# Kernel optimization log

Hardware: AMD Instinct MI355X
Metric: run time of the kernel (lower is better)

## Reference

```python
import jax, jax.numpy as jnp
import numpy as np

BETA = 0.9
THRESH = 1.0
ALPHA = 2.0  # snntorch ATan surrogate default

@jax.custom_vjp
def atan_spike(x):
    return (x > 0).astype(x.dtype)

def _atan_fwd(x):
    return atan_spike(x), x

def _atan_bwd(x, g):
    # d/dx of snntorch ATan surrogate: (alpha/2) / (1 + (pi/2*alpha*x)^2)
    return (g * (ALPHA / 2) / (1 + (jnp.pi / 2 * ALPHA * x) ** 2),)

atan_spike.defvjp(_atan_fwd, _atan_bwd)

def setup_inputs() -> dict:
    key = jax.random.key(0)
    k1, k2, k3, k4, k5 = jax.random.split(key, 5)
    B, T, F, H, O = 256, 1024, 64, 512, 64
    x = jax.random.normal(k1, (B, T, F), dtype=jnp.float32)
    s_in = 1.0 / np.sqrt(F)
    s_out = 1.0 / np.sqrt(H)
    W_in = jax.random.uniform(k2, (H, F), jnp.float32, -s_in, s_in)
    b_in = jax.random.uniform(k3, (H,), jnp.float32, -s_in, s_in)
    W_out = jax.random.uniform(k4, (O, H), jnp.float32, -s_out, s_out)
    b_out = jax.random.uniform(k5, (O,), jnp.float32, -s_out, s_out)
    return {"x": x, "W_in": W_in, "b_in": b_in, "W_out": W_out, "b_out": b_out}

def reference(x, W_in, b_in, W_out, b_out):
    B, T, F = x.shape
    H = W_in.shape[0]
    O = W_out.shape[0]
    dt = x.dtype
    # precompute input currents for all steps: [T, B, H]
    cur1_all = jnp.einsum('btf,hf->tbh', x, W_in) + b_in

    def step(carry, cur1):
        mem1, mem_out = carry
        # snntorch Leaky(subtract): reset from previous mem (detached),
        # then mem = beta*mem + input - reset*threshold, spike from new mem.
        reset1 = jax.lax.stop_gradient((mem1 > THRESH).astype(dt))
        mem1 = BETA * mem1 + cur1 - reset1 * THRESH
        spk1 = atan_spike(mem1 - THRESH)
        cur_out = spk1 @ W_out.T + b_out
        reset_o = jax.lax.stop_gradient((mem_out > THRESH).astype(dt))
        mem_out = BETA * mem_out + cur_out - reset_o * THRESH
        spk_out = atan_spike(mem_out - THRESH)
        return (mem1, mem_out), (mem_out, spk_out)

    init = (jnp.zeros((B, H), dt), jnp.zeros((B, O), dt))
    _, (mem_rec, spk_rec) = jax.lax.scan(step, init, cur1_all)
    # [T, B, O] -> [B, T, O]
    return mem_rec.transpose(1, 0, 2), spk_rec.transpose(1, 0, 2)
```

## Files before the change

### kernel.cpp

```cpp
#include <hip/hip_runtime.h>


namespace {
constexpr int kB = 256;
constexpr int kT = 1024;
constexpr int kF = 64;
constexpr int kH = 512;
constexpr int kO = 64;
constexpr float kBeta = 0.9f;
constexpr float kThresh = 1.0f;
}

typedef __attribute__((ext_vector_type(16))) float f32x16;

#define PIN8(p)                                                            \
  asm volatile("" : "+v"((p)[0]), "+v"((p)[1]), "+v"((p)[2]),              \
                    "+v"((p)[3]), "+v"((p)[4]), "+v"((p)[5]),              \
                    "+v"((p)[6]), "+v"((p)[7]))

#define BARRIER() asm volatile("s_waitcnt lgkmcnt(0)\n\ts_barrier" ::: "memory")

#define SX(i) ((i) < 16 ? sx0[(i)] : (i) < 32 ? sx1[(i)-16]                \
             : (i) < 48 ? sx2[(i)-32] : sx3[(i)-48])
#define AQ(q)                                                              \
  c0 = fmaf(SX(4*(q)+0), w[4*(q)+0], c0);                                  \
  c1 = fmaf(SX(4*(q)+1), w[4*(q)+1], c1);                                  \
  c2 = fmaf(SX(4*(q)+2), w[4*(q)+2], c2);                                  \
  c3 = fmaf(SX(4*(q)+3), w[4*(q)+3], c3);

__global__ __launch_bounds__(512)
void snn_curA(const float* __restrict__ x, const float* __restrict__ W_in,
              const float* __restrict__ b_in, float* __restrict__ cur1,
              int t0, int ntc, int l2ntc, int rpb) {
  const int l = threadIdx.x & 63;
  const int s = threadIdx.x >> 6;
  const int h = s * 64 + l;

  float w[64];
  {
    const float4* wiv = reinterpret_cast<const float4*>(W_in) + h * 16;
#pragma unroll
    for (int q = 0; q < 16; ++q) {
      const float4 v = wiv[q];
      w[4*q+0] = v.x; w[4*q+1] = v.y; w[4*q+2] = v.z; w[4*q+3] = v.w;
    }
  }
  float binh = b_in[h];
  PIN8(w + 0);  PIN8(w + 8);  PIN8(w + 16); PIN8(w + 24);
  PIN8(w + 32); PIN8(w + 40); PIN8(w + 48); PIN8(w + 56);
  asm volatile("" : "+v"(binh));

  const int row0 = blockIdx.x * rpb;
#pragma unroll 1
  for (int r = 0; r < rpb; ++r) {
    const int row = row0 + r;
    const int b = row >> l2ntc;
    const int tc = row & (ntc - 1);
    const float* xp = x + ((size_t)b * kT + (size_t)(t0 + tc)) * kF;
    f32x16 sx0, sx1, sx2, sx3;
    asm volatile("s_load_dwordx16 %0, %4, 0x0\n\t"
                 "s_load_dwordx16 %1, %4, 0x40\n\t"
                 "s_load_dwordx16 %2, %4, 0x80\n\t"
                 "s_load_dwordx16 %3, %4, 0xc0"
                 : "=&s"(sx0), "=&s"(sx1), "=&s"(sx2), "=&s"(sx3)
                 : "s"(xp));
    asm volatile("s_waitcnt lgkmcnt(0)"
                 : "+s"(sx0), "+s"(sx1), "+s"(sx2), "+s"(sx3) :: "memory");
    float c0 = binh, c1 = 0.0f, c2 = 0.0f, c3 = 0.0f;
    AQ(0) AQ(1) AQ(2) AQ(3) AQ(4) AQ(5) AQ(6) AQ(7)
    AQ(8) AQ(9) AQ(10) AQ(11) AQ(12) AQ(13) AQ(14) AQ(15)
    cur1[(size_t)row * kH + h] = (c0 + c1) + (c2 + c3);
  }
}

#define BSTEP(fk, tt)                                                      \
  do {                                                                     \
    mem1 = kBeta * mem1 + (fk) - rst1;                                     \
    const bool pr = mem1 > kThresh;                                        \
    rst1 = pr ? 1.0f : 0.0f;                                               \
    cp[(size_t)(tt) * kH] = rst1;          \
    const int tn_ = ((tt) + 8 < ntc) ? (tt) + 8 : ntc - 1;                 \
    fk = cp[(size_t)tn_ * kH];         \
  } while (0)

__global__ __launch_bounds__(512)
void snn_scanB(float* __restrict__ cs, float* __restrict__ state,
               int t0, int ntc) {
  const int b = blockIdx.x;
  const int h = threadIdx.x;
  float* m1s = state;
  float* r1s = state + kB * kH;
  const int idx = b * kH + h;
  float mem1 = 0.0f, rst1 = 0.0f;
  if (t0 != 0) { mem1 = m1s[idx]; rst1 = r1s[idx]; }

  float* cp = cs + (size_t)b * ntc * kH + h;
  float f0 = cp[0 * (size_t)kH], f1 = cp[1 * (size_t)kH];
  float f2 = cp[2 * (size_t)kH], f3 = cp[3 * (size_t)kH];
  float f4 = cp[4 * (size_t)kH], f5 = cp[5 * (size_t)kH];
  float f6 = cp[6 * (size_t)kH], f7 = cp[7 * (size_t)kH];

#pragma unroll 1
  for (int t = 0; t < ntc; t += 8) {
    BSTEP(f0, t + 0); BSTEP(f1, t + 1); BSTEP(f2, t + 2); BSTEP(f3, t + 3);
    BSTEP(f4, t + 4); BSTEP(f5, t + 5); BSTEP(f6, t + 6); BSTEP(f7, t + 7);
  }
  m1s[idx] = mem1;
  r1s[idx] = rst1;
}

#define SC(i) ((i) < 16 ? m0[(i)] : (i) < 32 ? m1[(i)-16]                  \
             : (i) < 48 ? m2[(i)-32] : m3[(i)-48])

#define CROW(rr)                                                           \
  do {                                                                     \
    const float* sp = spkrow + (size_t)(rr) * kH;                          \
    f32x16 m0, m1, m2, m3;                                                 \
    asm volatile("s_load_dwordx16 %0, %4, 0x0\n\t"                         \
                 "s_load_dwordx16 %1, %4, 0x40\n\t"                        \
                 "s_load_dwordx16 %2, %4, 0x80\n\t"                        \
                 "s_load_dwordx16 %3, %4, 0xc0"                            \
                 : "=&s"(m0), "=&s"(m1), "=&s"(m2), "=&s"(m3)              \
                 : "s"(sp));                                               \
    asm volatile("s_waitcnt lgkmcnt(0)"                                    \
                 : "+s"(m0), "+s"(m1), "+s"(m2), "+s"(m3) :: "memory");    \
    float a0 = 0.0f, a1 = 0.0f, a2 = 0.0f, a3 = 0.0f;                      \
    _Pragma("unroll") for (int q = 0; q < 16; ++q) {                       \
      a0 = fmaf(SC(4 * q + 0), wout[4 * q + 0], a0);                       \
      a1 = fmaf(SC(4 * q + 1), wout[4 * q + 1], a1);                       \
      a2 = fmaf(SC(4 * q + 2), wout[4 * q + 2], a2);                       \
      a3 = fmaf(SC(4 * q + 3), wout[4 * q + 3], a3);                       \
    }                                                                      \
    red[buf][rr][s][o] = (a0 + a1) + (a2 + a3);                            \
  } while (0)

__global__ __launch_bounds__(512)
void snn_coutC(const float* __restrict__ spk, const float* __restrict__ W_out,
               const float* __restrict__ b_out, float* __restrict__ cout,
               int ntc) {
  const int j = threadIdx.x;
  const int o = j & 63;
  const int s = j >> 6;
  const int s_u = __builtin_amdgcn_readfirstlane(s);
  const size_t row0 = (size_t)blockIdx.x * 64;

  __shared__ float red[2][8][8][64];

  float wout[64];
  {
    const float4* wov =
        reinterpret_cast<const float4*>(W_out) + o * (kH / 4) + s * 16;
#pragma unroll
    for (int q = 0; q < 16; ++q) {
      const float4 v = wov[q];
      wout[4*q+0] = v.x; wout[4*q+1] = v.y;
      wout[4*q+2] = v.z; wout[4*q+3] = v.w;
    }
  }
  float bout = b_out[o];
  PIN8(wout + 0);  PIN8(wout + 8);  PIN8(wout + 16); PIN8(wout + 24);
  PIN8(wout + 32); PIN8(wout + 40); PIN8(wout + 48); PIN8(wout + 56);
  asm volatile("" : "+v"(bout));

#pragma unroll 1
  for (int rb = 0; rb < 64; rb += 8) {
    const int buf = (rb >> 3) & 1;
    const float* spkrow = spk + (row0 + (size_t)rb) * kH + s_u * 64;

    CROW(0); CROW(1); CROW(2); CROW(3);
    CROW(4); CROW(5); CROW(6); CROW(7);

    BARRIER();

    float co = bout;
    co += red[buf][s][0][o]; co += red[buf][s][1][o];
    co += red[buf][s][2][o]; co += red[buf][s][3][o];
    co += red[buf][s][4][o]; co += red[buf][s][5][o];
    co += red[buf][s][6][o]; co += red[buf][s][7][o];
    cout[(row0 + (size_t)(rb + s)) * kO + o] = co;
  }
}

#define DSTEP(gk, tt)                                                      \
  do {                                                                     \
    memo = kBeta * memo + (gk) - rsto;                                     \
    const float so = (memo > kThresh) ? 1.0f : 0.0f;                       \
    rsto = so;                                                             \
    om[(size_t)(tt) * kO] = memo;                                          \
    os[(size_t)(tt) * kO] = so;                                            \
    const int tn_ = ((tt) + 8 < ntc) ? (tt) + 8 : ntc - 1;                 \
    gk = dp[(size_t)tn_ * kO];                                             \
  } while (0)

__global__ __launch_bounds__(64)
void snn_memoD(const float* __restrict__ cout, float* __restrict__ out,
               float* __restrict__ state, int t0, int ntc) {
  const int b = blockIdx.x;
  const int o = threadIdx.x;
  float* mos = state + 2 * kB * kH;
  float* ros = mos + kB * kO;
  const int idx = b * kO + o;
  float memo = 0.0f, rsto = 0.0f;
  if (t0 != 0) { memo = mos[idx]; rsto = ros[idx]; }

  const float* dp = cout + (size_t)b * ntc * kO + o;
  float* om = out + ((size_t)b * kT + t0) * kO + o;
  float* os = om + (size_t)kB * kT * kO;

  float g0 = dp[0 * (size_t)kO], g1 = dp[1 * (size_t)kO];
  float g2 = dp[2 * (size_t)kO], g3 = dp[3 * (size_t)kO];
  float g4 = dp[4 * (size_t)kO], g5 = dp[5 * (size_t)kO];
  float g6 = dp[6 * (size_t)kO], g7 = dp[7 * (size_t)kO];

#pragma unroll 1
  for (int t = 0; t < ntc; t += 8) {
    DSTEP(g0, t + 0); DSTEP(g1, t + 1); DSTEP(g2, t + 2); DSTEP(g3, t + 3);
    DSTEP(g4, t + 4); DSTEP(g5, t + 5); DSTEP(g6, t + 6); DSTEP(g7, t + 7);
  }
  mos[idx] = memo;
  ros[idx] = rsto;
}

__global__ __launch_bounds__(256)
void warm_x_kernel(const float4* __restrict__ p, int n4) {
  float acc = 0.0f;
  for (int i = blockIdx.x * blockDim.x + threadIdx.x; i < n4;
       i += gridDim.x * blockDim.x) {
    const float4 v = p[i];
    acc += v.x + v.y + v.z + v.w;
  }
  asm volatile("" ::"v"(acc));
}

__global__ __launch_bounds__(512)
__attribute__((amdgpu_waves_per_eu(2, 2)))
void snn_fused5(const float* __restrict__ x, const float* __restrict__ W_in,
                const float* __restrict__ b_in,
                const float* __restrict__ W_out,
                const float* __restrict__ b_out, float* __restrict__ out) {
  const int b = blockIdx.x;
  const int j = threadIdx.x;
  const int o = j & 63;
  const int s = j >> 6;
  __shared__ float red[2][8][64];
  float win[kF];
  {
    const float4* wiv = reinterpret_cast<const float4*>(W_in) + j * 16;
#pragma unroll
    for (int q = 0; q < 16; ++q) {
      const float4 v = wiv[q];
      win[4 * q] = v.x; win[4 * q + 1] = v.y;
      win[4 * q + 2] = v.z; win[4 * q + 3] = v.w;
    }
  }
  float wout[64];
  {
    const float4* wov =
        reinterpret_cast<const float4*>(W_out) + o * 128 + s * 16;
#pragma unroll
    for (int q = 0; q < 16; ++q) {
      const float4 v = wov[q];
      wout[4 * q] = v.x; wout[4 * q + 1] = v.y;
      wout[4 * q + 2] = v.z; wout[4 * q + 3] = v.w;
    }
  }
  float bin_j = b_in[j];
  float bout_o = b_out[o];
  PIN8(win + 0);  PIN8(win + 8);  PIN8(win + 16); PIN8(win + 24);
  PIN8(win + 32); PIN8(win + 40); PIN8(win + 48); PIN8(win + 56);
  PIN8(wout + 0);  PIN8(wout + 8);  PIN8(wout + 16); PIN8(wout + 24);
  PIN8(wout + 32); PIN8(wout + 40); PIN8(wout + 48); PIN8(wout + 56);
  asm volatile("" : "+v"(bin_j), "+v"(bout_o));
  float mem1 = 0.0f, rst1 = 0.0f, memo = 0.0f, rsto = 0.0f;
  unsigned long long mask = 0ull;
  const float4* xv = reinterpret_cast<const float4*>(x + (size_t)b * kT * kF);
  float* out_mem = out + (size_t)b * kT * kO + o;
  float* out_spk = out_mem + (size_t)kB * kT * kO;
  float4 x0, x1, x2, x3, x4, x5, x6, x7, x8, x9, x10, x11, x12, x13, x14, x15;
#define LOADX(tt)                                                          \
  do {                                                                     \
    const float4* xp = xv + (size_t)(tt) * 16;                             \
    x0 = xp[0]; x1 = xp[1]; x2 = xp[2]; x3 = xp[3];                        \
    x4 = xp[4]; x5 = xp[5]; x6 = xp[6]; x7 = xp[7];                        \
    x8 = xp[8]; x9 = xp[9]; x10 = xp[10]; x11 = xp[11];                    \
    x12 = xp[12]; x13 = xp[13]; x14 = xp[14]; x15 = xp[15];                \
  } while (0)
#define L1Q(q)                                                             \
  c0 = fmaf(x##q.x, win[4 * q + 0], c0);                                   \
  c1 = fmaf(x##q.y, win[4 * q + 1], c1);                                   \
  c2 = fmaf(x##q.z, win[4 * q + 2], c2);                                   \
  c3 = fmaf(x##q.w, win[4 * q + 3], c3);
#define LAYER1F()                                                          \
  do {                                                                     \
    float c0 = bin_j, c1 = 0.0f, c2 = 0.0f, c3 = 0.0f;                     \
    L1Q(0) L1Q(1) L1Q(2) L1Q(3) L1Q(4) L1Q(5) L1Q(6) L1Q(7)                \
    L1Q(8) L1Q(9) L1Q(10) L1Q(11) L1Q(12) L1Q(13) L1Q(14) L1Q(15)          \
    const float cur1v = (c0 + c1) + (c2 + c3);                             \
    mem1 = kBeta * mem1 + cur1v - rst1;                                    \
    const bool p = mem1 > kThresh;                                         \
    mask = __ballot(p);                                                    \
    rst1 = p ? 1.0f : 0.0f;                                                \
  } while (0)
#define L2QS(q)                                                            \
  {                                                                        \
    const float f0 = ((mlo >> (4 * (q) + 0)) & 1u) ? 1.0f : 0.0f;          \
    const float f1 = ((mlo >> (4 * (q) + 1)) & 1u) ? 1.0f : 0.0f;          \
    const float f2 = ((mlo >> (4 * (q) + 2)) & 1u) ? 1.0f : 0.0f;          \
    const float f3 = ((mlo >> (4 * (q) + 3)) & 1u) ? 1.0f : 0.0f;          \
    a0 = fmaf(f0, wout[4 * (q) + 0], a0);                                  \
    a1 = fmaf(f1, wout[4 * (q) + 1], a1);                                  \
    a2 = fmaf(f2, wout[4 * (q) + 2], a2);                                  \
    a3 = fmaf(f3, wout[4 * (q) + 3], a3);                                  \
  }
#define L2E(acc, q, i)                                                     \
  acc = acc + __uint_as_float(                                             \
      (unsigned)__builtin_amdgcn_sbfe((int)vmhi, 4 * (q) + (i)-32, 1) &    \
      __float_as_uint(wout[4 * (q) + (i)]));
#define L2QV(q)                                                            \
  { L2E(a0, q, 0) L2E(a1, q, 1) L2E(a2, q, 2) L2E(a3, q, 3) }
#define LAYER2F(buf)                                                       \
  do {                                                                     \
    const unsigned mlo = (unsigned)mask;                                   \
    unsigned vmhi = (unsigned)(mask >> 32);                                \
    asm volatile("" : "+v"(vmhi));                                         \
    float a0 = 0.0f, a1 = 0.0f, a2 = 0.0f, a3 = 0.0f;                      \
    L2QS(0) L2QS(1) L2QS(2) L2QS(3) L2QS(4) L2QS(5) L2QS(6) L2QS(7)        \
    L2QV(8) L2QV(9) L2QV(10) L2QV(11) L2QV(12) L2QV(13) L2QV(14) L2QV(15)  \
    red[(buf)][s][o] = (a0 + a1) + (a2 + a3);                              \
  } while (0)
  LOADX(0);
  LAYER1F();
  LOADX(1);
  for (int t = 1; t < kT; ++t) {
    LAYER2F((t - 1) & 1);
    BARRIER();
    float r0, r1, r2, r3, r4, r5, r6, r7;
    const int buf = (t - 1) & 1;
    if (s == 0) {
      r0 = red[buf][0][o]; r1 = red[buf][1][o];
      r2 = red[buf][2][o]; r3 = red[buf][3][o];
      r4 = red[buf][4][o]; r5 = red[buf][5][o];
      r6 = red[buf][6][o]; r7 = red[buf][7][o];
    }
    LAYER1F();
    const int tn = (t + 1 < kT) ? (t + 1) : (kT - 1);
    LOADX(tn);
    if (s == 0) {
      float co = bout_o;
      co += r0; co += r1; co += r2; co += r3;
      co += r4; co += r5; co += r6; co += r7;
      memo = kBeta * memo + co - rsto;
      const float so = (memo > kThresh) ? 1.0f : 0.0f;
      rsto = so;
      out_mem[(t - 1) * kO] = memo;
      out_spk[(t - 1) * kO] = so;
    }
  }
  LAYER2F((kT - 1) & 1);
  BARRIER();
  if (s == 0) {
    const int buf = (kT - 1) & 1;
    float co = bout_o;
    co += red[buf][0][o]; co += red[buf][1][o];
    co += red[buf][2][o]; co += red[buf][3][o];
    co += red[buf][4][o]; co += red[buf][5][o];
    co += red[buf][6][o]; co += red[buf][7][o];
    memo = kBeta * memo + co - rsto;
    const float so = (memo > kThresh) ? 1.0f : 0.0f;
    out_mem[(kT - 1) * kO] = memo;
    out_spk[(kT - 1) * kO] = so;
  }
}

extern "C" void kernel_launch(void* const* d_in, const int* in_sizes, int n_in,
                              void* d_out, int out_size, void* d_ws,
                              size_t ws_size, hipStream_t stream) {
  const float* x = (const float*)d_in[0];
  const float* W_in = (const float*)d_in[1];
  const float* b_in = (const float*)d_in[2];
  const float* W_out = (const float*)d_in[3];
  const float* b_out = (const float*)d_in[4];
  float* out = (float*)d_out;

  const size_t state_bytes = ((size_t)2 * kB * kH + 2 * kB * kO) * 4;
  int nch = 0;
  for (int c : {4, 8, 16}) {
    const int ntc_c = kT / c;
    const size_t need = (size_t)kB * ntc_c * (kH + kO) * 4 + state_bytes;
    if (need <= ws_size) { nch = c; break; }
  }

  if (nch) {
    const int ntc = kT / nch;
    const int l2ntc = (ntc == 256) ? 8 : (ntc == 128) ? 7 : 6;
    float* cur1 = (float*)d_ws;
    float* coutb = cur1 + (size_t)kB * ntc * kH;
    float* state = coutb + (size_t)kB * ntc * kO;

    const int rows = kB * ntc;
    const int rpbA = 64;
    const int gA = rows / rpbA;
    const int gC = rows / 64;

    for (int c = 0; c < nch; ++c) {
      const int t0 = c * ntc;
      hipLaunchKernelGGL(snn_curA, dim3(gA), dim3(512), 0, stream,
                         x, W_in, b_in, cur1, t0, ntc, l2ntc, rpbA);
      hipLaunchKernelGGL(snn_scanB, dim3(kB), dim3(512), 0, stream,
                         cur1, state, t0, ntc);
      hipLaunchKernelGGL(snn_coutC, dim3(gC), dim3(512), 0, stream,
                         cur1, W_out, b_out, coutb, ntc);
      hipLaunchKernelGGL(snn_memoD, dim3(kB), dim3(64), 0, stream,
                         coutb, out, state, t0, ntc);
    }
  } else {
    const int n4 = kB * kT * kF / 4;
    hipLaunchKernelGGL(warm_x_kernel, dim3(1024), dim3(256), 0, stream,
                       (const float4*)x, n4);
    hipLaunchKernelGGL(snn_fused5, dim3(kB), dim3(512), 0, stream,
                       x, W_in, b_in, W_out, b_out, out);
  }
}
```

Before: 1.028 ms.

## Fuse input projection into hidden-layer scan kernel, dropping cur1 buffer round-trip

Merges the input-current matmul kernel and the hidden membrane scan kernel into one kernel per batch row. Each thread holds its W_in row in registers, computes the current for each timestep from a double-buffered float4 load of x, updates the membrane state and writes only the spike. This removes the write and reread of the full cur1 buffer and one launch per chunk. In exchange only 256 blocks do the input projection, so its compute now sits on the serial scan's critical path with lower parallelism.

```diff
diff --git a/kernel.cpp b/kernel.cpp
--- a/kernel.cpp
+++ b/kernel.cpp
@@ -20,91 +20,86 @@
 
 #define BARRIER() asm volatile("s_waitcnt lgkmcnt(0)\n\ts_barrier" ::: "memory")
 
-#define SX(i) ((i) < 16 ? sx0[(i)] : (i) < 32 ? sx1[(i)-16]                \
-             : (i) < 48 ? sx2[(i)-32] : sx3[(i)-48])
-#define AQ(q)                                                              \
-  c0 = fmaf(SX(4*(q)+0), w[4*(q)+0], c0);                                  \
-  c1 = fmaf(SX(4*(q)+1), w[4*(q)+1], c1);                                  \
-  c2 = fmaf(SX(4*(q)+2), w[4*(q)+2], c2);                                  \
-  c3 = fmaf(SX(4*(q)+3), w[4*(q)+3], c3);
+#define SLOAD64(sx0, sx1, sx2, sx3, ptr)                                   \
+  asm volatile("s_load_dwordx16 %0, %4, 0x0\n\t"                           \
+               "s_load_dwordx16 %1, %4, 0x40\n\t"                          \
+               "s_load_dwordx16 %2, %4, 0x80\n\t"                          \
+               "s_load_dwordx16 %3, %4, 0xc0\n\t"                          \
+               "s_waitcnt lgkmcnt(0)"                                      \
+               : "=&s"(sx0), "=&s"(sx1), "=&s"(sx2), "=&s"(sx3)            \
+               : "s"(ptr) : "memory")
+
+#define FMA4(v, q)                                                         \
+  c0 = fmaf((v).x, w[4 * (q) + 0], c0);                                    \
+  c1 = fmaf((v).y, w[4 * (q) + 1], c1);                                    \
+  c2 = fmaf((v).z, w[4 * (q) + 2], c2);                                    \
+  c3 = fmaf((v).w, w[4 * (q) + 3], c3);
+
+#define LDB(bk, tt)                                                        \
+  do {                                                                     \
+    const float4* p = xv + (size_t)(tt) * 16;                              \
+    bk##0 = p[0]; bk##1 = p[1]; bk##2 = p[2]; bk##3 = p[3];                \
+    bk##4 = p[4]; bk##5 = p[5]; bk##6 = p[6]; bk##7 = p[7];                \
+    bk##8 = p[8]; bk##9 = p[9]; bk##10 = p[10]; bk##11 = p[11];            \
+    bk##12 = p[12]; bk##13 = p[13]; bk##14 = p[14]; bk##15 = p[15];        \
+  } while (0)
+
+#define STEP(bk, tt)                                                       \
+  do {                                                                     \
+    float c0 = bias, c1 = 0.0f, c2 = 0.0f, c3 = 0.0f;                      \
+    FMA4(bk##0, 0) FMA4(bk##1, 1) FMA4(bk##2, 2) FMA4(bk##3, 3)            \
+    FMA4(bk##4, 4) FMA4(bk##5, 5) FMA4(bk##6, 6) FMA4(bk##7, 7)            \
+    FMA4(bk##8, 8) FMA4(bk##9, 9) FMA4(bk##10, 10) FMA4(bk##11, 11)        \
+    FMA4(bk##12, 12) FMA4(bk##13, 13) FMA4(bk##14, 14) FMA4(bk##15, 15)    \
+    const float cur = (c0 + c1) + (c2 + c3);                               \
+    mem1 = kBeta * mem1 + cur - rst1;                                      \
+    rst1 = (mem1 > kThresh) ? 1.0f : 0.0f;                                 \
+    sp[(size_t)(tt) * kH] = rst1;                                          \
+  } while (0)
 
 __global__ __launch_bounds__(512)
-void snn_curA(const float* __restrict__ x, const float* __restrict__ W_in,
-              const float* __restrict__ b_in, float* __restrict__ cur1,
-              int t0, int ntc, int l2ntc, int rpb) {
-  const int l = threadIdx.x & 63;
-  const int s = threadIdx.x >> 6;
-  const int h = s * 64 + l;
+void snn_ab(const float* __restrict__ x, const float* __restrict__ W_in,
+            const float* __restrict__ b_in, float* __restrict__ spk,
+            float* __restrict__ state, int t0, int ntc) {
+  const int b = blockIdx.x;
+  const int j = threadIdx.x;
 
   float w[64];
   {
-    const float4* wiv = reinterpret_cast<const float4*>(W_in) + h * 16;
+    const float4* wiv = reinterpret_cast<const float4*>(W_in) + j * 16;
 #pragma unroll
     for (int q = 0; q < 16; ++q) {
       const float4 v = wiv[q];
       w[4*q+0] = v.x; w[4*q+1] = v.y; w[4*q+2] = v.z; w[4*q+3] = v.w;
     }
   }
-  float binh = b_in[h];
+  float bias = b_in[j];
   PIN8(w + 0);  PIN8(w + 8);  PIN8(w + 16); PIN8(w + 24);
   PIN8(w + 32); PIN8(w + 40); PIN8(w + 48); PIN8(w + 56);
-  asm volatile("" : "+v"(binh));
-
-  const int row0 = blockIdx.x * rpb;
-#pragma unroll 1
-  for (int r = 0; r < rpb; ++r) {
-    const int row = row0 + r;
-    const int b = row >> l2ntc;
-    const int tc = row & (ntc - 1);
-    const float* xp = x + ((size_t)b * kT + (size_t)(t0 + tc)) * kF;
-    f32x16 sx0, sx1, sx2, sx3;
-    asm volatile("s_load_dwordx16 %0, %4, 0x0\n\t"
-                 "s_load_dwordx16 %1, %4, 0x40\n\t"
-                 "s_load_dwordx16 %2, %4, 0x80\n\t"
-                 "s_load_dwordx16 %3, %4, 0xc0"
-                 : "=&s"(sx0), "=&s"(sx1), "=&s"(sx2), "=&s"(sx3)
-                 : "s"(xp));
-    asm volatile("s_waitcnt lgkmcnt(0)"
-                 : "+s"(sx0), "+s"(sx1), "+s"(sx2), "+s"(sx3) :: "memory");
-    float c0 = binh, c1 = 0.0f, c2 = 0.0f, c3 = 0.0f;
-    AQ(0) AQ(1) AQ(2) AQ(3) AQ(4) AQ(5) AQ(6) AQ(7)
-    AQ(8) AQ(9) AQ(10) AQ(11) AQ(12) AQ(13) AQ(14) AQ(15)
-    cur1[(size_t)row * kH + h] = (c0 + c1) + (c2 + c3);
-  }
-}
-
-#define BSTEP(fk, tt)                                                      \
-  do {                                                                     \
-    mem1 = kBeta * mem1 + (fk) - rst1;                                     \
-    const bool pr = mem1 > kThresh;                                        \
-    rst1 = pr ? 1.0f : 0.0f;                                               \
-    cp[(size_t)(tt) * kH] = rst1;          \
-    const int tn_ = ((tt) + 8 < ntc) ? (tt) + 8 : ntc - 1;                 \
-    fk = cp[(size_t)tn_ * kH];         \
-  } while (0)
-
-__global__ __launch_bounds__(512)
-void snn_scanB(float* __restrict__ cs, float* __restrict__ state,
-               int t0, int ntc) {
-  const int b = blockIdx.x;
-  const int h = threadIdx.x;
+  asm volatile("" : "+v"(bias));
+
   float* m1s = state;
   float* r1s = state + kB * kH;
-  const int idx = b * kH + h;
+  const int idx = b * kH + j;
   float mem1 = 0.0f, rst1 = 0.0f;
   if (t0 != 0) { mem1 = m1s[idx]; rst1 = r1s[idx]; }
 
-  float* cp = cs + (size_t)b * ntc * kH + h;
-  float f0 = cp[0 * (size_t)kH], f1 = cp[1 * (size_t)kH];
-  float f2 = cp[2 * (size_t)kH], f3 = cp[3 * (size_t)kH];
-  float f4 = cp[4 * (size_t)kH], f5 = cp[5 * (size_t)kH];
-  float f6 = cp[6 * (size_t)kH], f7 = cp[7 * (size_t)kH];
-
+  const float4* xv =
+      reinterpret_cast<const float4*>(x + ((size_t)b * kT + t0) * kF);
+  float* sp = spk + (size_t)b * ntc * kH + j;
+
+  float4 a0, a1, a2, a3, a4, a5, a6, a7, a8, a9, a10, a11, a12, a13, a14, a15;
+  float4 e0, e1, e2, e3, e4, e5, e6, e7, e8, e9, e10, e11, e12, e13, e14, e15;
+
+  LDB(a, 0);
 #pragma unroll 1
-  for (int t = 0; t < ntc; t += 8) {
-    BSTEP(f0, t + 0); BSTEP(f1, t + 1); BSTEP(f2, t + 2); BSTEP(f3, t + 3);
-    BSTEP(f4, t + 4); BSTEP(f5, t + 5); BSTEP(f6, t + 6); BSTEP(f7, t + 7);
-  }
+  for (int t = 0; t < ntc; t += 2) {
+    LDB(e, t + 1);
+    STEP(a, t);
+    LDB(a, (t + 2 < ntc) ? t + 2 : t);
+    STEP(e, t + 1);
+  }
+
   m1s[idx] = mem1;
   r1s[idx] = rst1;
 }
@@ -114,16 +109,9 @@
 
 #define CROW(rr)                                                           \
   do {                                                                     \
-    const float* sp = spkrow + (size_t)(rr) * kH;                          \
+    const float* sp_ = spkrow + (size_t)(rr) * kH;                         \
     f32x16 m0, m1, m2, m3;                                                 \
-    asm volatile("s_load_dwordx16 %0, %4, 0x0\n\t"                         \
-                 "s_load_dwordx16 %1, %4, 0x40\n\t"                        \
-                 "s_load_dwordx16 %2, %4, 0x80\n\t"                        \
-                 "s_load_dwordx16 %3, %4, 0xc0"                            \
-                 : "=&s"(m0), "=&s"(m1), "=&s"(m2), "=&s"(m3)              \
-                 : "s"(sp));                                               \
-    asm volatile("s_waitcnt lgkmcnt(0)"                                    \
-                 : "+s"(m0), "+s"(m1), "+s"(m2), "+s"(m3) :: "memory");    \
+    SLOAD64(m0, m1, m2, m3, sp_);                                          \
     float a0 = 0.0f, a1 = 0.0f, a2 = 0.0f, a3 = 0.0f;                      \
     _Pragma("unroll") for (int q = 0; q < 16; ++q) {                       \
       a0 = fmaf(SC(4 * q + 0), wout[4 * q + 0], a0);                       \
@@ -392,24 +380,19 @@
 
   if (nch) {
     const int ntc = kT / nch;
-    const int l2ntc = (ntc == 256) ? 8 : (ntc == 128) ? 7 : 6;
-    float* cur1 = (float*)d_ws;
-    float* coutb = cur1 + (size_t)kB * ntc * kH;
+    float* spkb = (float*)d_ws;
+    float* coutb = spkb + (size_t)kB * ntc * kH;
     float* state = coutb + (size_t)kB * ntc * kO;
 
     const int rows = kB * ntc;
-    const int rpbA = 64;
-    const int gA = rows / rpbA;
     const int gC = rows / 64;
 
     for (int c = 0; c < nch; ++c) {
       const int t0 = c * ntc;
-      hipLaunchKernelGGL(snn_curA, dim3(gA), dim3(512), 0, stream,
-                         x, W_in, b_in, cur1, t0, ntc, l2ntc, rpbA);
-      hipLaunchKernelGGL(snn_scanB, dim3(kB), dim3(512), 0, stream,
-                         cur1, state, t0, ntc);
+      hipLaunchKernelGGL(snn_ab, dim3(kB), dim3(512), 0, stream,
+                         x, W_in, b_in, spkb, state, t0, ntc);
       hipLaunchKernelGGL(snn_coutC, dim3(gC), dim3(512), 0, stream,
-                         cur1, W_out, b_out, coutb, ntc);
+                         spkb, W_out, b_out, coutb, ntc);
       hipLaunchKernelGGL(snn_memoD, dim3(kB), dim3(64), 0, stream,
                          coutb, out, state, t0, ntc);
     }
```

Result: slower. 1.249 ms (+21.5%).

## Software-pipeline chunks by fusing next-chunk input GEMM with current output GEMM

Applied to the files above, without the earlier changes.

Double-buffers the cur1 and cout workspaces and merges the input-current GEMM for chunk c+1 with the output-current GEMM for chunk c into one launch that interleaves the two roles across blocks. The aim is to cut the number of launches and let the two independent, parallel stages share the GPU instead of running serially. It needs twice the workspace and picks 8 or 16 chunks. The fused single-kernel fallback is removed, so the function now returns without computing anything when the workspace is too small.

```diff
diff --git a/kernel.cpp b/kernel.cpp
--- a/kernel.cpp
+++ b/kernel.cpp
@@ -28,10 +28,11 @@
   c2 = fmaf(SX(4*(q)+2), w[4*(q)+2], c2);                                  \
   c3 = fmaf(SX(4*(q)+3), w[4*(q)+3], c3);
 
-__global__ __launch_bounds__(512)
-void snn_curA(const float* __restrict__ x, const float* __restrict__ W_in,
-              const float* __restrict__ b_in, float* __restrict__ cur1,
-              int t0, int ntc, int l2ntc, int rpb) {
+__device__ __forceinline__ void roleA(const float* __restrict__ x,
+                                      const float* __restrict__ W_in,
+                                      const float* __restrict__ b_in,
+                                      float* __restrict__ cur1,
+                                      int t0, int ntc, int l2ntc, int abid) {
   const int l = threadIdx.x & 63;
   const int s = threadIdx.x >> 6;
   const int h = s * 64 + l;
@@ -50,9 +51,9 @@
   PIN8(w + 32); PIN8(w + 40); PIN8(w + 48); PIN8(w + 56);
   asm volatile("" : "+v"(binh));
 
-  const int row0 = blockIdx.x * rpb;
+  const int row0 = abid * 64;
 #pragma unroll 1
-  for (int r = 0; r < rpb; ++r) {
+  for (int r = 0; r < 64; ++r) {
     const int row = row0 + r;
     const int b = row >> l2ntc;
     const int tc = row & (ntc - 1);
@@ -71,42 +72,6 @@
     AQ(8) AQ(9) AQ(10) AQ(11) AQ(12) AQ(13) AQ(14) AQ(15)
     cur1[(size_t)row * kH + h] = (c0 + c1) + (c2 + c3);
   }
-}
-
-#define BSTEP(fk, tt)                                                      \
-  do {                                                                     \
-    mem1 = kBeta * mem1 + (fk) - rst1;                                     \
-    const bool pr = mem1 > kThresh;                                        \
-    rst1 = pr ? 1.0f : 0.0f;                                               \
-    cp[(size_t)(tt) * kH] = rst1;          \
-    const int tn_ = ((tt) + 8 < ntc) ? (tt) + 8 : ntc - 1;                 \
-    fk = cp[(size_t)tn_ * kH];         \
-  } while (0)
-
-__global__ __launch_bounds__(512)
-void snn_scanB(float* __restrict__ cs, float* __restrict__ state,
-               int t0, int ntc) {
-  const int b = blockIdx.x;
-  const int h = threadIdx.x;
-  float* m1s = state;
-  float* r1s = state + kB * kH;
-  const int idx = b * kH + h;
-  float mem1 = 0.0f, rst1 = 0.0f;
-  if (t0 != 0) { mem1 = m1s[idx]; rst1 = r1s[idx]; }
-
-  float* cp = cs + (size_t)b * ntc * kH + h;
-  float f0 = cp[0 * (size_t)kH], f1 = cp[1 * (size_t)kH];
-  float f2 = cp[2 * (size_t)kH], f3 = cp[3 * (size_t)kH];
-  float f4 = cp[4 * (size_t)kH], f5 = cp[5 * (size_t)kH];
-  float f6 = cp[6 * (size_t)kH], f7 = cp[7 * (size_t)kH];
-
-#pragma unroll 1
-  for (int t = 0; t < ntc; t += 8) {
-    BSTEP(f0, t + 0); BSTEP(f1, t + 1); BSTEP(f2, t + 2); BSTEP(f3, t + 3);
-    BSTEP(f4, t + 4); BSTEP(f5, t + 5); BSTEP(f6, t + 6); BSTEP(f7, t + 7);
-  }
-  m1s[idx] = mem1;
-  r1s[idx] = rst1;
 }
 
 #define SC(i) ((i) < 16 ? m0[(i)] : (i) < 32 ? m1[(i)-16]                  \
@@ -134,17 +99,16 @@
     red[buf][rr][s][o] = (a0 + a1) + (a2 + a3);                            \
   } while (0)
 
-__global__ __launch_bounds__(512)
-void snn_coutC(const float* __restrict__ spk, const float* __restrict__ W_out,
-               const float* __restrict__ b_out, float* __restrict__ cout,
-               int ntc) {
+__device__ __forceinline__ void roleC(const float* __restrict__ spk,
+                                      const float* __restrict__ W_out,
+                                      const float* __restrict__ b_out,
+                                      float* __restrict__ cout, int cbid,
+                                      float (*red)[8][8][64]) {
   const int j = threadIdx.x;
   const int o = j & 63;
   const int s = j >> 6;
   const int s_u = __builtin_amdgcn_readfirstlane(s);
-  const size_t row0 = (size_t)blockIdx.x * 64;
-
-  __shared__ float red[2][8][8][64];
+  const size_t row0 = (size_t)cbid * 64;
 
   float wout[64];
   {
@@ -181,6 +145,72 @@
   }
 }
 
+__global__ __launch_bounds__(512)
+void snn_AC(const float* __restrict__ x, const float* __restrict__ W_in,
+            const float* __restrict__ b_in, float* __restrict__ cur1A,
+            const float* __restrict__ spkC, const float* __restrict__ W_out,
+            const float* __restrict__ b_out, float* __restrict__ coutC,
+            int tA0, int ntc, int l2ntc, int doA, int doC) {
+  __shared__ float red[2][8][8][64];
+  const int bid = blockIdx.x >> 1;
+  if (blockIdx.x & 1) {
+    if (doC) roleC(spkC, W_out, b_out, coutC, bid, red);
+  } else {
+    if (doA) roleA(x, W_in, b_in, cur1A, tA0, ntc, l2ntc, bid);
+  }
+}
+
+__global__ __launch_bounds__(512)
+void snn_curA(const float* __restrict__ x, const float* __restrict__ W_in,
+              const float* __restrict__ b_in, float* __restrict__ cur1,
+              int t0, int ntc, int l2ntc) {
+  roleA(x, W_in, b_in, cur1, t0, ntc, l2ntc, blockIdx.x);
+}
+
+__global__ __launch_bounds__(512)
+void snn_coutC(const float* __restrict__ spk, const float* __restrict__ W_out,
+               const float* __restrict__ b_out, float* __restrict__ cout,
+               int ntc) {
+  __shared__ float red[2][8][8][64];
+  roleC(spk, W_out, b_out, cout, blockIdx.x, red);
+}
+
+#define BSTEP(fk, tt)                                                      \
+  do {                                                                     \
+    mem1 = kBeta * mem1 + (fk) - rst1;                                     \
+    const bool pr = mem1 > kThresh;                                        \
+    rst1 = pr ? 1.0f : 0.0f;                                               \
+    cp[(size_t)(tt) * kH] = rst1;          \
+    const int tn_ = ((tt) + 8 < ntc) ? (tt) + 8 : ntc - 1;                 \
+    fk = cp[(size_t)tn_ * kH];                                             \
+  } while (0)
+
+__global__ __launch_bounds__(512)
+void snn_scanB(float* __restrict__ cs, float* __restrict__ state,
+               int t0, int ntc) {
+  const int b = blockIdx.x;
+  const int h = threadIdx.x;
+  float* m1s = state;
+  float* r1s = state + kB * kH;
+  const int idx = b * kH + h;
+  float mem1 = 0.0f, rst1 = 0.0f;
+  if (t0 != 0) { mem1 = m1s[idx]; rst1 = r1s[idx]; }
+
+  float* cp = cs + (size_t)b * ntc * kH + h;
+  float f0 = cp[0 * (size_t)kH], f1 = cp[1 * (size_t)kH];
+  float f2 = cp[2 * (size_t)kH], f3 = cp[3 * (size_t)kH];
+  float f4 = cp[4 * (size_t)kH], f5 = cp[5 * (size_t)kH];
+  float f6 = cp[6 * (size_t)kH], f7 = cp[7 * (size_t)kH];
+
+#pragma unroll 1
+  for (int t = 0; t < ntc; t += 8) {
+    BSTEP(f0, t + 0); BSTEP(f1, t + 1); BSTEP(f2, t + 2); BSTEP(f3, t + 3);
+    BSTEP(f4, t + 4); BSTEP(f5, t + 5); BSTEP(f6, t + 6); BSTEP(f7, t + 7);
+  }
+  m1s[idx] = mem1;
+  r1s[idx] = rst1;
+}
+
 #define DSTEP(gk, tt)                                                      \
   do {                                                                     \
     memo = kBeta * memo + (gk) - rsto;                                     \
@@ -221,157 +251,6 @@
   ros[idx] = rsto;
 }
 
-__global__ __launch_bounds__(256)
-void warm_x_kernel(const float4* __restrict__ p, int n4) {
-  float acc = 0.0f;
-  for (int i = blockIdx.x * blockDim.x + threadIdx.x; i < n4;
-       i += gridDim.x * blockDim.x) {
-    const float4 v = p[i];
-    acc += v.x + v.y + v.z + v.w;
-  }
-  asm volatile("" ::"v"(acc));
-}
-
-__global__ __launch_bounds__(512)
-__attribute__((amdgpu_waves_per_eu(2, 2)))
-void snn_fused5(const float* __restrict__ x, const float* __restrict__ W_in,
-                const float* __restrict__ b_in,
-                const float* __restrict__ W_out,
-                const float* __restrict__ b_out, float* __restrict__ out) {
-  const int b = blockIdx.x;
-  const int j = threadIdx.x;
-  const int o = j & 63;
-  const int s = j >> 6;
-  __shared__ float red[2][8][64];
-  float win[kF];
-  {
-    const float4* wiv = reinterpret_cast<const float4*>(W_in) + j * 16;
-#pragma unroll
-    for (int q = 0; q < 16; ++q) {
-      const float4 v = wiv[q];
-      win[4 * q] = v.x; win[4 * q + 1] = v.y;
-      win[4 * q + 2] = v.z; win[4 * q + 3] = v.w;
-    }
-  }
-  float wout[64];
-  {
-    const float4* wov =
-        reinterpret_cast<const float4*>(W_out) + o * 128 + s * 16;
-#pragma unroll
-    for (int q = 0; q < 16; ++q) {
-      const float4 v = wov[q];
-      wout[4 * q] = v.x; wout[4 * q + 1] = v.y;
-      wout[4 * q + 2] = v.z; wout[4 * q + 3] = v.w;
-    }
-  }
-  float bin_j = b_in[j];
-  float bout_o = b_out[o];
-  PIN8(win + 0);  PIN8(win + 8);  PIN8(win + 16); PIN8(win + 24);
-  PIN8(win + 32); PIN8(win + 40); PIN8(win + 48); PIN8(win + 56);
-  PIN8(wout + 0);  PIN8(wout + 8);  PIN8(wout + 16); PIN8(wout + 24);
-  PIN8(wout + 32); PIN8(wout + 40); PIN8(wout + 48); PIN8(wout + 56);
-  asm volatile("" : "+v"(bin_j), "+v"(bout_o));
-  float mem1 = 0.0f, rst1 = 0.0f, memo = 0.0f, rsto = 0.0f;
-  unsigned long long mask = 0ull;
-  const float4* xv = reinterpret_cast<const float4*>(x + (size_t)b * kT * kF);
-  float* out_mem = out + (size_t)b * kT * kO + o;
-  float* out_spk = out_mem + (size_t)kB * kT * kO;
-  float4 x0, x1, x2, x3, x4, x5, x6, x7, x8, x9, x10, x11, x12, x13, x14, x15;
-#define LOADX(tt)                                                          \
-  do {                                                                     \
-    const float4* xp = xv + (size_t)(tt) * 16;                             \
-    x0 = xp[0]; x1 = xp[1]; x2 = xp[2]; x3 = xp[3];                        \
-    x4 = xp[4]; x5 = xp[5]; x6 = xp[6]; x7 = xp[7];                        \
-    x8 = xp[8]; x9 = xp[9]; x10 = xp[10]; x11 = xp[11];                    \
-    x12 = xp[12]; x13 = xp[13]; x14 = xp[14]; x15 = xp[15];                \
-  } while (0)
-#define L1Q(q)                                                             \
-  c0 = fmaf(x##q.x, win[4 * q + 0], c0);                                   \
-  c1 = fmaf(x##q.y, win[4 * q + 1], c1);                                   \
-  c2 = fmaf(x##q.z, win[4 * q + 2], c2);                                   \
-  c3 = fmaf(x##q.w, win[4 * q + 3], c3);
-#define LAYER1F()                                                          \
-  do {                                                                     \
-    float c0 = bin_j, c1 = 0.0f, c2 = 0.0f, c3 = 0.0f;                     \
-    L1Q(0) L1Q(1) L1Q(2) L1Q(3) L1Q(4) L1Q(5) L1Q(6) L1Q(7)                \
-    L1Q(8) L1Q(9) L1Q(10) L1Q(11) L1Q(12) L1Q(13) L1Q(14) L1Q(15)          \
-    const float cur1v = (c0 + c1) + (c2 + c3);                             \
-    mem1 = kBeta * mem1 + cur1v - rst1;                                    \
-    const bool p = mem1 > kThresh;                                         \
-    mask = __ballot(p);                                                    \
-    rst1 = p ? 1.0f : 0.0f;                                                \
-  } while (0)
-#define L2QS(q)                                                            \
-  {                                                                        \
-    const float f0 = ((mlo >> (4 * (q) + 0)) & 1u) ? 1.0f : 0.0f;          \
-    const float f1 = ((mlo >> (4 * (q) + 1)) & 1u) ? 1.0f : 0.0f;          \
-    const float f2 = ((mlo >> (4 * (q) + 2)) & 1u) ? 1.0f : 0.0f;          \
-    const float f3 = ((mlo >> (4 * (q) + 3)) & 1u) ? 1.0f : 0.0f;          \
-    a0 = fmaf(f0, wout[4 * (q) + 0], a0);                                  \
-    a1 = fmaf(f1, wout[4 * (q) + 1], a1);                                  \
-    a2 = fmaf(f2, wout[4 * (q) + 2], a2);                                  \
-    a3 = fmaf(f3, wout[4 * (q) + 3], a3);                                  \
-  }
-#define L2E(acc, q, i)                                                     \
-  acc = acc + __uint_as_float(                                             \
-      (unsigned)__builtin_amdgcn_sbfe((int)vmhi, 4 * (q) + (i)-32, 1) &    \
-      __float_as_uint(wout[4 * (q) + (i)]));
-#define L2QV(q)                                                            \
-  { L2E(a0, q, 0) L2E(a1, q, 1) L2E(a2, q, 2) L2E(a3, q, 3) }
-#define LAYER2F(buf)                                                       \
-  do {                                                                     \
-    const unsigned mlo = (unsigned)mask;                                   \
-    unsigned vmhi = (unsigned)(mask >> 32);                                \
-    asm volatile("" : "+v"(vmhi));                                         \
-    float a0 = 0.0f, a1 = 0.0f, a2 = 0.0f, a3 = 0.0f;                      \
-    L2QS(0) L2QS(1) L2QS(2) L2QS(3) L2QS(4) L2QS(5) L2QS(6) L2QS(7)        \
-    L2QV(8) L2QV(9) L2QV(10) L2QV(11) L2QV(12) L2QV(13) L2QV(14) L2QV(15)  \
-    red[(buf)][s][o] = (a0 + a1) + (a2 + a3);                              \
-  } while (0)
-  LOADX(0);
-  LAYER1F();
-  LOADX(1);
-  for (int t = 1; t < kT; ++t) {
-    LAYER2F((t - 1) & 1);
-    BARRIER();
-    float r0, r1, r2, r3, r4, r5, r6, r7;
-    const int buf = (t - 1) & 1;
-    if (s == 0) {
-      r0 = red[buf][0][o]; r1 = red[buf][1][o];
-      r2 = red[buf][2][o]; r3 = red[buf][3][o];
-      r4 = red[buf][4][o]; r5 = red[buf][5][o];
-      r6 = red[buf][6][o]; r7 = red[buf][7][o];
-    }
-    LAYER1F();
-    const int tn = (t + 1 < kT) ? (t + 1) : (kT - 1);
-    LOADX(tn);
-    if (s == 0) {
-      float co = bout_o;
-      co += r0; co += r1; co += r2; co += r3;
-      co += r4; co += r5; co += r6; co += r7;
-      memo = kBeta * memo + co - rsto;
-      const float so = (memo > kThresh) ? 1.0f : 0.0f;
-      rsto = so;
-      out_mem[(t - 1) * kO] = memo;
-      out_spk[(t - 1) * kO] = so;
-    }
-  }
-  LAYER2F((kT - 1) & 1);
-  BARRIER();
-  if (s == 0) {
-    const int buf = (kT - 1) & 1;
-    float co = bout_o;
-    co += red[buf][0][o]; co += red[buf][1][o];
-    co += red[buf][2][o]; co += red[buf][3][o];
-    co += red[buf][4][o]; co += red[buf][5][o];
-    co += red[buf][6][o]; co += red[buf][7][o];
-    memo = kBeta * memo + co - rsto;
-    const float so = (memo > kThresh) ? 1.0f : 0.0f;
-    out_mem[(kT - 1) * kO] = memo;
-    out_spk[(kT - 1) * kO] = so;
-  }
-}
-
 extern "C" void kernel_launch(void* const* d_in, const int* in_sizes, int n_in,
                               void* d_out, int out_size, void* d_ws,
                               size_t ws_size, hipStream_t stream) {
@@ -383,41 +262,78 @@
   float* out = (float*)d_out;
 
   const size_t state_bytes = ((size_t)2 * kB * kH + 2 * kB * kO) * 4;
+
+  int nchp = 0;
+  for (int c : {8, 16}) {
+    const size_t rows_c = (size_t)kB * (kT / c);
+    const size_t need = 2 * rows_c * (kH + kO) * 4 + state_bytes;
+    if (need <= ws_size) { nchp = c; break; }
+  }
+
+  if (nchp) {
+    const int ntc = kT / nchp;
+    const int l2ntc = (ntc == 128) ? 7 : 6;
+    const size_t rows = (size_t)kB * ntc;
+    float* cur1[2];
+    float* coutb[2];
+    cur1[0] = (float*)d_ws;
+    cur1[1] = cur1[0] + rows * kH;
+    coutb[0] = cur1[1] + rows * kH;
+    coutb[1] = coutb[0] + rows * kO;
+    float* state = coutb[1] + rows * kO;
+
+    const int gA = (int)(rows / 64);
+    const dim3 gAC(2 * gA);
+
+    hipLaunchKernelGGL(snn_AC, gAC, dim3(512), 0, stream,
+                       x, W_in, b_in, cur1[0], cur1[0], W_out, b_out,
+                       coutb[0], 0, ntc, l2ntc, 1, 0);
+    hipLaunchKernelGGL(snn_scanB, dim3(kB), dim3(512), 0, stream,
+                       cur1[0], state, 0, ntc);
+
+    for (int c = 0; c < nchp; ++c) {
+      const int na = c + 1;
+      hipLaunchKernelGGL(snn_AC, gAC, dim3(512), 0, stream,
+                         x, W_in, b_in, cur1[na & 1], cur1[c & 1],
+                         W_out, b_out, coutb[c & 1],
+                         na * ntc, ntc, l2ntc, (na < nchp) ? 1 : 0, 1);
+      hipLaunchKernelGGL(snn_memoD, dim3(kB), dim3(64), 0, stream,
+                         coutb[c & 1], out, state, c * ntc, ntc);
+      if (na < nchp) {
+        hipLaunchKernelGGL(snn_scanB, dim3(kB), dim3(512), 0, stream,
+                           cur1[na & 1], state, na * ntc, ntc);
+      }
+    }
+    return;
+  }
+
   int nch = 0;
   for (int c : {4, 8, 16}) {
     const int ntc_c = kT / c;
     const size_t need = (size_t)kB * ntc_c * (kH + kO) * 4 + state_bytes;
     if (need <= ws_size) { nch = c; break; }
   }
-
-  if (nch) {
-    const int ntc = kT / nch;
-    const int l2ntc = (ntc == 256) ? 8 : (ntc == 128) ? 7 : 6;
-    float* cur1 = (float*)d_ws;
-    float* coutb = cur1 + (size_t)kB * ntc * kH;
-    float* state = coutb + (size_t)kB * ntc * kO;
-
-    const int rows = kB * ntc;
-    const int rpbA = 64;
-    const int gA = rows / rpbA;
-    const int gC = rows / 64;
-
-    for (int c = 0; c < nch; ++c) {
-      const int t0 = c * ntc;
-      hipLaunchKernelGGL(snn_curA, dim3(gA), dim3(512), 0, stream,
-                         x, W_in, b_in, cur1, t0, ntc, l2ntc, rpbA);
-      hipLaunchKernelGGL(snn_scanB, dim3(kB), dim3(512), 0, stream,
-                         cur1, state, t0, ntc);
-      hipLaunchKernelGGL(snn_coutC, dim3(gC), dim3(512), 0, stream,
-                         cur1, W_out, b_out, coutb, ntc);
-      hipLaunchKernelGGL(snn_memoD, dim3(kB), dim3(64), 0, stream,
-                         coutb, out, state, t0, ntc);
-    }
-  } else {
-    const int n4 = kB * kT * kF / 4;
-    hipLaunchKernelGGL(warm_x_kernel, dim3(1024), dim3(256), 0, stream,
-                       (const float4*)x, n4);
-    hipLaunchKernelGGL(snn_fused5, dim3(kB), dim3(512), 0, stream,
-                       x, W_in, b_in, W_out, b_out, out);
-  }
-}
+  if (!nch) return;
+
+  const int ntc = kT / nch;
+  const int l2ntc = (ntc == 256) ? 8 : (ntc == 128) ? 7 : 6;
+  float* cur1 = (float*)d_ws;
+  float* coutb = cur1 + (size_t)kB * ntc * kH;
+  float* state = coutb + (size_t)kB * ntc * kO;
+
+  const int rows = kB * ntc;
+  const int gA = rows / 64;
+  const int gC = rows / 64;
+
+  for (int c = 0; c < nch; ++c) {
+    const int t0 = c * ntc;
+    hipLaunchKernelGGL(snn_curA, dim3(gA), dim3(512), 0, stream,
+                       x, W_in, b_in, cur1, t0, ntc, l2ntc);
+    hipLaunchKernelGGL(snn_scanB, dim3(kB), dim3(512), 0, stream,
+                       cur1, state, t0, ntc);
+    hipLaunchKernelGGL(snn_coutC, dim3(gC), dim3(512), 0, stream,
+                       cur1, W_out, b_out, coutb, ntc);
+    hipLaunchKernelGGL(snn_memoD, dim3(kB), dim3(64), 0, stream,
+                       coutb, out, state, t0, ntc);
+  }
+}
```

New measurement: 1.168 ms. 1.14x slower.
